# Optimization experiments

Measured on AMD Instinct MI355X. Metric: run time of the kernel, lower is better.

The kernel has to match this reference:

```python
import jax, jax.numpy as jnp
import numpy as np

NEG = -9.0e15


def setup_inputs() -> dict:
    key = jax.random.key(0)
    k_x, k_w, k_e, k_b, k_m = jax.random.split(key, 5)
    B, N, C, F = 2048, 64, 256, 256
    x = jax.random.normal(k_x, (B, N, C), dtype=jnp.float32)
    W = jax.random.normal(k_w, (2, C, F), dtype=jnp.float32) * (1.414 / np.sqrt(C + F))
    # full logit tensor; only entries where mask holds are ever read (equivalent
    # to torch's flat `e` scattered into the nonzero positions of adj)
    e = jax.random.normal(k_e, (F, N, N), dtype=jnp.float32)
    bias = jax.random.normal(k_b, (F,), dtype=jnp.float32) * (1.0 / np.sqrt(C))
    # symmetric adjacency mask with self-loops, density ~0.3
    m = jax.random.bernoulli(k_m, 0.3, (N, N))
    mask = (m | m.T) | jnp.eye(N, dtype=bool)
    return {"x": x, "W": W, "e": e, "bias": bias, "mask": mask}


def reference(x, W, e, bias, mask):
    # x: [B,N,C], W: [2,C,F], e: [F,N,N], bias: [F], mask: [N,N] bool
    h0 = x @ W[0]                                   # [B,N,F] (self term)
    h1 = x @ W[1]                                   # [B,N,F] (neighbor term)
    logits = jnp.where(mask[None, :, :], e, NEG)    # [F,N,N]
    adj = jax.nn.softmax(logits, axis=2)            # per-channel row softmax
    N = mask.shape[0]
    eye = jnp.eye(N, dtype=bool)
    d = jnp.diagonal(adj, axis1=1, axis2=2)         # [F,N]  (adj * E diagonal)
    off = jnp.where(eye[None, :, :], 0.0, adj)      # [F,N,N] (adj * (1-E))
    # (adj*E) @ h0 reduces to per-node diagonal scaling; off-diag is a
    # per-channel NxN matmul batched over B.
    out = d.T[None, :, :] * h0 + jnp.einsum('fnm,bmf->bnf', off, h1)
    return out + bias[None, None, :]
```

## Files before the change

### kernel.cpp

```cpp
#include <hip/hip_runtime.h>
#include <hip/hip_bf16.h>


typedef __attribute__((ext_vector_type(8))) short  fragA;
typedef __attribute__((ext_vector_type(4))) float  f32x4;
typedef __attribute__((ext_vector_type(8))) unsigned short u16x8;
typedef __attribute__((ext_vector_type(4))) unsigned short u16x4;

constexpr long OFF_OFF = 0;
constexpr long OFF_WT  = 2l * 1024 * 1024;
constexpr long OFF_DS  = OFF_WT + 512l * 256 * 2;
constexpr long OFF_H1  = OFF_DS + 64l * 256 * 4;
constexpr long WS_NEED = OFF_H1 + 256l * 131072 * 2;

static __device__ inline unsigned short f2bf(float f) {
  __hip_bfloat16 h = __float2bfloat16(f);
  return __builtin_bit_cast(unsigned short, h);
}
static __device__ inline float bf2f(unsigned short u) {
  unsigned int x = ((unsigned int)u) << 16;
  return __builtin_bit_cast(float, x);
}

__global__ __launch_bounds__(256) void k_prep(const float* __restrict__ e,
                                              const unsigned char* __restrict__ mask,
                                              char* __restrict__ ws_b) {
  unsigned short* off = (unsigned short*)(ws_b + OFF_OFF);
  float* dscale = (float*)(ws_b + OFF_DS);
  const int lane = threadIdx.x & 63;
  const int row  = blockIdx.x * 4 + (threadIdx.x >> 6);
  const int f = row >> 6, n = row & 63;

  bool is_u8 = __all(mask[lane * 65] != 0);
  bool mv;
  if (is_u8) mv = mask[n * 64 + lane] != 0;
  else       mv = ((const int*)mask)[n * 64 + lane] != 0;

  float v = mv ? e[(long)row * 64 + lane] : -1e30f;
  float mx = v;
#pragma unroll
  for (int s = 32; s; s >>= 1) mx = fmaxf(mx, __shfl_xor(mx, s));
  float ex = mv ? __expf(v - mx) : 0.f;
  float sm = ex;
#pragma unroll
  for (int s = 32; s; s >>= 1) sm += __shfl_xor(sm, s);
  float adj = ex / sm;
  if (lane == n) dscale[n * 256 + f] = adj;
  off[(long)row * 64 + lane] = f2bf(lane == n ? 0.f : adj);
}

__global__ __launch_bounds__(256) void k_wt(const float* __restrict__ W,
                                            char* __restrict__ ws_b) {
  unsigned short* Wt = (unsigned short*)(ws_b + OFF_WT);
  __shared__ float t[64][65];
  const int bid = blockIdx.x;
  const int w = bid >> 4, f0 = ((bid >> 2) & 3) * 64, c0 = (bid & 3) * 64;
  const int tr = threadIdx.x >> 2, tc = (threadIdx.x & 3) * 16;
  const float* src = W + ((long)(w * 256 + c0 + tr)) * 256 + f0 + tc;
#pragma unroll
  for (int i = 0; i < 16; i += 4) {
    float4 v = *(const float4*)(src + i);
    t[tr][tc + i] = v.x; t[tr][tc + i + 1] = v.y;
    t[tr][tc + i + 2] = v.z; t[tr][tc + i + 3] = v.w;
  }
  __syncthreads();
  u16x8 p0, p1;
#pragma unroll
  for (int i = 0; i < 8; i++)  p0[i] = f2bf(t[tc + i][tr]);
#pragma unroll
  for (int i = 0; i < 8; i++)  p1[i] = f2bf(t[tc + 8 + i][tr]);
  unsigned short* dst = Wt + ((long)(w * 256 + f0 + tr)) * 256 + c0 + tc;
  *(u16x8*)dst = p0;
  *(u16x8*)(dst + 8) = p1;
}

__global__ __launch_bounds__(512) void k_gemm(const float* __restrict__ x,
                                              const float* __restrict__ bias,
                                              char* __restrict__ ws_b,
                                              float* __restrict__ out) {
  const unsigned short* Wt = (const unsigned short*)(ws_b + OFF_WT);
  const float* dscale = (const float*)(ws_b + OFF_DS);
  __shared__ __align__(16) unsigned short smem[256 * 136];
  unsigned short* As = smem;
  unsigned short* Bs = smem + 128 * 72;

  const int tid  = threadIdx.x;
  const int bcol = blockIdx.x;
  const long R0  = (long)blockIdx.y * 128;
  const int wid  = tid >> 6, lane = tid & 63;
  const int wr = wid & 1, wc = wid >> 1;
  const int lr = lane & 15, lkb = (lane >> 4) * 8;

  f32x4 acc[4][4] = {};

  for (int k0 = 0; k0 < 256; k0 += 64) {
    {
      int r = tid >> 2, cb = (tid & 3) * 16;
      const float* src = x + (R0 + r) * 256 + k0 + cb;
      float4 v0 = ((const float4*)src)[0];
      float4 v1 = ((const float4*)src)[1];
      float4 v2 = ((const float4*)src)[2];
      float4 v3 = ((const float4*)src)[3];
      u16x8 p0, p1;
      p0[0]=f2bf(v0.x); p0[1]=f2bf(v0.y); p0[2]=f2bf(v0.z); p0[3]=f2bf(v0.w);
      p0[4]=f2bf(v1.x); p0[5]=f2bf(v1.y); p0[6]=f2bf(v1.z); p0[7]=f2bf(v1.w);
      p1[0]=f2bf(v2.x); p1[1]=f2bf(v2.y); p1[2]=f2bf(v2.z); p1[3]=f2bf(v2.w);
      p1[4]=f2bf(v3.x); p1[5]=f2bf(v3.y); p1[6]=f2bf(v3.z); p1[7]=f2bf(v3.w);
      unsigned short* d = As + r * 72 + cb;
      *(u16x8*)d = p0;
      *(u16x8*)(d + 8) = p1;
    }
    {
      int j = tid >> 1, cb = (tid & 1) * 32;
      const unsigned short* src = Wt + ((long)(bcol * 256 + j)) * 256 + k0 + cb;
      unsigned short* d = Bs + j * 72 + cb;
      *(u16x8*)(d)      = *(const u16x8*)(src);
      *(u16x8*)(d + 8)  = *(const u16x8*)(src + 8);
      *(u16x8*)(d + 16) = *(const u16x8*)(src + 16);
      *(u16x8*)(d + 24) = *(const u16x8*)(src + 24);
    }
    __syncthreads();
#pragma unroll
    for (int kk = 0; kk < 2; kk++) {
      fragA af[4], bfm[4];
#pragma unroll
      for (int i = 0; i < 4; i++)
        af[i] = *(const fragA*)(As + (wr * 64 + i * 16 + lr) * 72 + kk * 32 + lkb);
#pragma unroll
      for (int j = 0; j < 4; j++)
        bfm[j] = *(const fragA*)(Bs + (wc * 64 + j * 16 + lr) * 72 + kk * 32 + lkb);
#pragma unroll
      for (int i = 0; i < 4; i++)
#pragma unroll
        for (int j = 0; j < 4; j++)
          acc[i][j] = __builtin_amdgcn_mfma_f32_16x16x32_bf16(af[i], bfm[j], acc[i][j], 0, 0, 0);
    }
    __syncthreads();
  }

  if (bcol == 0) {
#pragma unroll
    for (int i = 0; i < 4; i++) {
#pragma unroll
      for (int j = 0; j < 4; j++) {
        int f = wc * 64 + j * 16 + lr;
        float bs = bias[f];
#pragma unroll
        for (int r = 0; r < 4; r++) {
          long R = R0 + wr * 64 + i * 16 + (lane >> 4) * 4 + r;
          int n = (int)(R & 63);
          out[R * 256 + f] = acc[i][j][r] * dscale[n * 256 + f] + bs;
        }
      }
    }
  } else {
    unsigned short* Ts = smem;
#pragma unroll
    for (int i = 0; i < 4; i++) {
#pragma unroll
      for (int j = 0; j < 4; j++) {
        int fl = wc * 64 + j * 16 + lr;
        int rb = wr * 64 + i * 16 + (lane >> 4) * 4;
        u16x4 pk;
        pk[0] = f2bf(acc[i][j][0]); pk[1] = f2bf(acc[i][j][1]);
        pk[2] = f2bf(acc[i][j][2]); pk[3] = f2bf(acc[i][j][3]);
        *(u16x4*)(Ts + fl * 136 + rb) = pk;
      }
    }
    __syncthreads();
    unsigned short* h1ws = (unsigned short*)(ws_b + OFF_H1);
    int fl = tid >> 1, rb2 = (tid & 1) * 64;
    unsigned short* dst = h1ws + (long)fl * 131072 + R0 + rb2;
    const unsigned short* s = Ts + fl * 136 + rb2;
#pragma unroll
    for (int i = 0; i < 8; i++)
      *(u16x8*)(dst + i * 8) = *(const u16x8*)(s + i * 8);
  }
}

__global__ __launch_bounds__(256) void k_einsum(char* __restrict__ ws_b,
                                                float* __restrict__ out) {
  const unsigned short* offp = (const unsigned short*)(ws_b + OFF_OFF);
  const unsigned short* h1ws = (const unsigned short*)(ws_b + OFF_H1);
  __shared__ __align__(16) unsigned short Ds[16 * 64 * 24];
  const int tid = threadIdx.x;
  const long B0 = (long)blockIdx.x * 16;
  const int f0 = blockIdx.y * 16;
  const int wid = tid >> 6, lane = tid & 63;
  const int lr = lane & 15, lkb = (lane >> 4) * 8;

  for (int q = 0; q < 4; q++) {
    int fi = wid * 4 + q;
    long f = f0 + fi;
    f32x4 acc[4] = {};
    const unsigned short* ha = h1ws + f * 131072 + (B0 + lr) * 64;
    const unsigned short* ob = offp + f * 4096;
#pragma unroll
    for (int kt = 0; kt < 2; kt++) {
      fragA a = *(const fragA*)(ha + kt * 32 + lkb);
#pragma unroll
      for (int ct = 0; ct < 4; ct++) {
        fragA b = *(const fragA*)(ob + (ct * 16 + lr) * 64 + kt * 32 + lkb);
        acc[ct] = __builtin_amdgcn_mfma_f32_16x16x32_bf16(a, b, acc[ct], 0, 0, 0);
      }
    }
#pragma unroll
    for (int ct = 0; ct < 4; ct++) {
      int n = ct * 16 + lr;
#pragma unroll
      for (int r = 0; r < 4; r++) {
        int b = (lane >> 4) * 4 + r;
        Ds[(b * 64 + n) * 24 + fi] = f2bf(acc[ct][r]);
      }
    }
  }
  __syncthreads();
#pragma unroll
  for (int i = 0; i < 4; i++) {
    int r = tid + 256 * i;
    float* o = out + (B0 * 64 + r) * 256 + f0;
    const unsigned short* ds = Ds + r * 24;
    u16x8 d0 = *(const u16x8*)(ds);
    u16x8 d1 = *(const u16x8*)(ds + 8);
    float4 o0 = ((float4*)o)[0], o1 = ((float4*)o)[1];
    float4 o2 = ((float4*)o)[2], o3 = ((float4*)o)[3];
    o0.x += bf2f(d0[0]); o0.y += bf2f(d0[1]); o0.z += bf2f(d0[2]); o0.w += bf2f(d0[3]);
    o1.x += bf2f(d0[4]); o1.y += bf2f(d0[5]); o1.z += bf2f(d0[6]); o1.w += bf2f(d0[7]);
    o2.x += bf2f(d1[0]); o2.y += bf2f(d1[1]); o2.z += bf2f(d1[2]); o2.w += bf2f(d1[3]);
    o3.x += bf2f(d1[4]); o3.y += bf2f(d1[5]); o3.z += bf2f(d1[6]); o3.w += bf2f(d1[7]);
    ((float4*)o)[0] = o0; ((float4*)o)[1] = o1;
    ((float4*)o)[2] = o2; ((float4*)o)[3] = o3;
  }
}

extern "C" void kernel_launch(void* const* d_in, const int* in_sizes, int n_in,
                              void* d_out, int out_size, void* d_ws, size_t ws_size,
                              hipStream_t stream) {
  const float* x    = (const float*)d_in[0];
  const float* W    = (const float*)d_in[1];
  const float* e    = (const float*)d_in[2];
  const float* bias = (const float*)d_in[3];
  const unsigned char* mask = (const unsigned char*)d_in[4];
  float* out = (float*)d_out;
  char* ws = (char*)d_ws;
  if (ws_size < (size_t)WS_NEED) return;

  k_prep<<<4096, 256, 0, stream>>>(e, mask, ws);
  k_wt<<<32, 256, 0, stream>>>(W, ws);
  dim3 g2(2, 1024);
  k_gemm<<<g2, 512, 0, stream>>>(x, bias, ws, out);
  dim3 g3(128, 16);
  k_einsum<<<g3, 256, 0, stream>>>(ws, out);
}
```

Baseline: 241.8 us.

## Fuse projection GEMM and per-channel einsum into one kernel keeping h1 in LDS

```diff
diff --git a/kernel.cpp b/kernel.cpp
--- a/kernel.cpp
+++ b/kernel.cpp
@@ -10,8 +10,7 @@
 constexpr long OFF_OFF = 0;
 constexpr long OFF_WT  = 2l * 1024 * 1024;
 constexpr long OFF_DS  = OFF_WT + 512l * 256 * 2;
-constexpr long OFF_H1  = OFF_DS + 64l * 256 * 4;
-constexpr long WS_NEED = OFF_H1 + 256l * 131072 * 2;
+constexpr long WS_NEED = OFF_DS + 64l * 256 * 4;
 
 static __device__ inline unsigned short f2bf(float f) {
   __hip_bfloat16 h = __float2bfloat16(f);
@@ -29,7 +28,7 @@
   float* dscale = (float*)(ws_b + OFF_DS);
   const int lane = threadIdx.x & 63;
   const int row  = blockIdx.x * 4 + (threadIdx.x >> 6);
-  const int f = row >> 6, n = row & 63;
+  const int n = row & 63;
 
   bool is_u8 = __all(mask[lane * 65] != 0);
   bool mv;
@@ -45,6 +44,7 @@
 #pragma unroll
   for (int s = 32; s; s >>= 1) sm += __shfl_xor(sm, s);
   float adj = ex / sm;
+  const int f = row >> 6;
   if (lane == n) dscale[n * 256 + f] = adj;
   off[(long)row * 64 + lane] = f2bf(lane == n ? 0.f : adj);
 }
@@ -74,162 +74,123 @@
   *(u16x8*)(dst + 8) = p1;
 }
 
-__global__ __launch_bounds__(512) void k_gemm(const float* __restrict__ x,
-                                              const float* __restrict__ bias,
-                                              char* __restrict__ ws_b,
-                                              float* __restrict__ out) {
-  const unsigned short* Wt = (const unsigned short*)(ws_b + OFF_WT);
-  const float* dscale = (const float*)(ws_b + OFF_DS);
-  __shared__ __align__(16) unsigned short smem[256 * 136];
-  unsigned short* As = smem;
-  unsigned short* Bs = smem + 128 * 72;
-
-  const int tid  = threadIdx.x;
-  const int bcol = blockIdx.x;
-  const long R0  = (long)blockIdx.y * 128;
-  const int wid  = tid >> 6, lane = tid & 63;
-  const int wr = wid & 1, wc = wid >> 1;
-  const int lr = lane & 15, lkb = (lane >> 4) * 8;
+__global__ __launch_bounds__(512, 4) void k_main(const float* __restrict__ x,
+                                                 const float* __restrict__ bias,
+                                                 const char* __restrict__ ws_b,
+                                                 float* __restrict__ out) {
+  const unsigned short* Wt   = (const unsigned short*)(ws_b + OFF_WT);
+  const unsigned short* offp = (const unsigned short*)(ws_b + OFF_OFF);
+  const float* dscale        = (const float*)(ws_b + OFF_DS);
+
+  __shared__ __align__(16) unsigned short Bs[64 * 264];
+  __shared__ __align__(16) unsigned short Hb[19264];
+
+  const int tid = threadIdx.x;
+  const int wid = tid >> 6, lane = tid & 63;
+  const int lr = lane & 15, hi = lane >> 4;
+
+  const int wg = blockIdx.x;
+  const int xcd = wg & 7, s = wg >> 3;
+  const int bb = xcd * 32 + (s >> 3);
+  const int fb = s & 7;
+  const int f0 = fb * 32;
+  const long R0 = (long)bb * 512;
+  const long Rw = R0 + wid * 64;
+
+  {
+    int c = tid >> 3, ch = (tid & 7) * 32;
+    int wrow = (c < 32) ? (f0 + c) : (256 + f0 + c - 32);
+    const unsigned short* src = Wt + (long)wrow * 256 + ch;
+    unsigned short* d = &Bs[c * 264 + ch];
+    *(u16x8*)(d)      = *(const u16x8*)(src);
+    *(u16x8*)(d + 8)  = *(const u16x8*)(src + 8);
+    *(u16x8*)(d + 16) = *(const u16x8*)(src + 16);
+    *(u16x8*)(d + 24) = *(const u16x8*)(src + 24);
+  }
+  __syncthreads();
 
   f32x4 acc[4][4] = {};
-
-  for (int k0 = 0; k0 < 256; k0 += 64) {
-    {
-      int r = tid >> 2, cb = (tid & 3) * 16;
-      const float* src = x + (R0 + r) * 256 + k0 + cb;
-      float4 v0 = ((const float4*)src)[0];
-      float4 v1 = ((const float4*)src)[1];
-      float4 v2 = ((const float4*)src)[2];
-      float4 v3 = ((const float4*)src)[3];
-      u16x8 p0, p1;
-      p0[0]=f2bf(v0.x); p0[1]=f2bf(v0.y); p0[2]=f2bf(v0.z); p0[3]=f2bf(v0.w);
-      p0[4]=f2bf(v1.x); p0[5]=f2bf(v1.y); p0[6]=f2bf(v1.z); p0[7]=f2bf(v1.w);
-      p1[0]=f2bf(v2.x); p1[1]=f2bf(v2.y); p1[2]=f2bf(v2.z); p1[3]=f2bf(v2.w);
-      p1[4]=f2bf(v3.x); p1[5]=f2bf(v3.y); p1[6]=f2bf(v3.z); p1[7]=f2bf(v3.w);
-      unsigned short* d = As + r * 72 + cb;
-      *(u16x8*)d = p0;
-      *(u16x8*)(d + 8) = p1;
-    }
-    {
-      int j = tid >> 1, cb = (tid & 1) * 32;
-      const unsigned short* src = Wt + ((long)(bcol * 256 + j)) * 256 + k0 + cb;
-      unsigned short* d = Bs + j * 72 + cb;
-      *(u16x8*)(d)      = *(const u16x8*)(src);
-      *(u16x8*)(d + 8)  = *(const u16x8*)(src + 8);
-      *(u16x8*)(d + 16) = *(const u16x8*)(src + 16);
-      *(u16x8*)(d + 24) = *(const u16x8*)(src + 24);
-    }
-    __syncthreads();
+#pragma unroll
+  for (int ks = 0; ks < 8; ks++) {
+    fragA af[4], bfr[4];
+#pragma unroll
+    for (int i = 0; i < 4; i++) {
+      const float* p = x + (Rw + i * 16 + lr) * 256 + ks * 32 + hi * 8;
+      float4 v0 = *(const float4*)p;
+      float4 v1 = *(const float4*)(p + 4);
+      u16x8 t;
+      t[0] = f2bf(v0.x); t[1] = f2bf(v0.y); t[2] = f2bf(v0.z); t[3] = f2bf(v0.w);
+      t[4] = f2bf(v1.x); t[5] = f2bf(v1.y); t[6] = f2bf(v1.z); t[7] = f2bf(v1.w);
+      af[i] = __builtin_bit_cast(fragA, t);
+    }
+#pragma unroll
+    for (int j = 0; j < 4; j++)
+      bfr[j] = *(const fragA*)&Bs[(j * 16 + lr) * 264 + ks * 32 + hi * 8];
+#pragma unroll
+    for (int i = 0; i < 4; i++)
+#pragma unroll
+      for (int j = 0; j < 4; j++)
+        acc[i][j] = __builtin_amdgcn_mfma_f32_16x16x32_bf16(af[i], bfr[j], acc[i][j], 0, 0, 0);
+  }
+
+#pragma unroll
+  for (int i = 0; i < 4; i++) {
+#pragma unroll
+    for (int j = 2; j < 4; j++) {
+      int fl = (j - 2) * 16 + lr;
+      int m  = i * 16 + hi * 4;
+      u16x4 pk;
+      pk[0] = f2bf(acc[i][j][0]); pk[1] = f2bf(acc[i][j][1]);
+      pk[2] = f2bf(acc[i][j][2]); pk[3] = f2bf(acc[i][j][3]);
+      *(u16x4*)&Hb[fl * 584 + wid * 72 + m] = pk;
+    }
+  }
+  __syncthreads();
+
+#pragma unroll
+  for (int q = 0; q < 4; q++) {
+    int fl = wid * 4 + q;
+    long fg = f0 + fl;
+    f32x4 ea[4] = {};
+    const unsigned short* ob = offp + fg * 4096;
 #pragma unroll
     for (int kk = 0; kk < 2; kk++) {
-      fragA af[4], bfm[4];
-#pragma unroll
-      for (int i = 0; i < 4; i++)
-        af[i] = *(const fragA*)(As + (wr * 64 + i * 16 + lr) * 72 + kk * 32 + lkb);
-#pragma unroll
-      for (int j = 0; j < 4; j++)
-        bfm[j] = *(const fragA*)(Bs + (wc * 64 + j * 16 + lr) * 72 + kk * 32 + lkb);
-#pragma unroll
-      for (int i = 0; i < 4; i++)
-#pragma unroll
-        for (int j = 0; j < 4; j++)
-          acc[i][j] = __builtin_amdgcn_mfma_f32_16x16x32_bf16(af[i], bfm[j], acc[i][j], 0, 0, 0);
-    }
-    __syncthreads();
-  }
-
-  if (bcol == 0) {
-#pragma unroll
-    for (int i = 0; i < 4; i++) {
-#pragma unroll
-      for (int j = 0; j < 4; j++) {
-        int f = wc * 64 + j * 16 + lr;
-        float bs = bias[f];
+      fragA a = *(const fragA*)&Hb[fl * 584 + lr * 72 + kk * 32 + hi * 8];
+#pragma unroll
+      for (int ct = 0; ct < 4; ct++) {
+        fragA b = *(const fragA*)(ob + (ct * 16 + lr) * 64 + kk * 32 + hi * 8);
+        ea[ct] = __builtin_amdgcn_mfma_f32_16x16x32_bf16(a, b, ea[ct], 0, 0, 0);
+      }
+    }
+    if (hi < 2) {
+#pragma unroll
+      for (int ct = 0; ct < 4; ct++) {
 #pragma unroll
         for (int r = 0; r < 4; r++) {
-          long R = R0 + wr * 64 + i * 16 + (lane >> 4) * 4 + r;
-          int n = (int)(R & 63);
-          out[R * 256 + f] = acc[i][j][r] * dscale[n * 256 + f] + bs;
+          int b = hi * 4 + r;
+          int n = ct * 16 + lr;
+          Hb[fl * 584 + b * 72 + n] = f2bf(ea[ct][r]);
         }
       }
     }
-  } else {
-    unsigned short* Ts = smem;
-#pragma unroll
-    for (int i = 0; i < 4; i++) {
-#pragma unroll
-      for (int j = 0; j < 4; j++) {
-        int fl = wc * 64 + j * 16 + lr;
-        int rb = wr * 64 + i * 16 + (lane >> 4) * 4;
-        u16x4 pk;
-        pk[0] = f2bf(acc[i][j][0]); pk[1] = f2bf(acc[i][j][1]);
-        pk[2] = f2bf(acc[i][j][2]); pk[3] = f2bf(acc[i][j][3]);
-        *(u16x4*)(Ts + fl * 136 + rb) = pk;
+  }
+  __syncthreads();
+
+#pragma unroll
+  for (int i = 0; i < 4; i++) {
+#pragma unroll
+    for (int j = 0; j < 2; j++) {
+      int fl = j * 16 + lr;
+      int f  = f0 + fl;
+      float bs = bias[f];
+#pragma unroll
+      for (int r = 0; r < 4; r++) {
+        int m = i * 16 + hi * 4 + r;
+        float ev = bf2f(Hb[fl * 584 + wid * 72 + m]);
+        long R = Rw + m;
+        out[R * 256 + f] = dscale[m * 256 + f] * acc[i][j][r] + ev + bs;
       }
     }
-    __syncthreads();
-    unsigned short* h1ws = (unsigned short*)(ws_b + OFF_H1);
-    int fl = tid >> 1, rb2 = (tid & 1) * 64;
-    unsigned short* dst = h1ws + (long)fl * 131072 + R0 + rb2;
-    const unsigned short* s = Ts + fl * 136 + rb2;
-#pragma unroll
-    for (int i = 0; i < 8; i++)
-      *(u16x8*)(dst + i * 8) = *(const u16x8*)(s + i * 8);
-  }
-}
-
-__global__ __launch_bounds__(256) void k_einsum(char* __restrict__ ws_b,
-                                                float* __restrict__ out) {
-  const unsigned short* offp = (const unsigned short*)(ws_b + OFF_OFF);
-  const unsigned short* h1ws = (const unsigned short*)(ws_b + OFF_H1);
-  __shared__ __align__(16) unsigned short Ds[16 * 64 * 24];
-  const int tid = threadIdx.x;
-  const long B0 = (long)blockIdx.x * 16;
-  const int f0 = blockIdx.y * 16;
-  const int wid = tid >> 6, lane = tid & 63;
-  const int lr = lane & 15, lkb = (lane >> 4) * 8;
-
-  for (int q = 0; q < 4; q++) {
-    int fi = wid * 4 + q;
-    long f = f0 + fi;
-    f32x4 acc[4] = {};
-    const unsigned short* ha = h1ws + f * 131072 + (B0 + lr) * 64;
-    const unsigned short* ob = offp + f * 4096;
-#pragma unroll
-    for (int kt = 0; kt < 2; kt++) {
-      fragA a = *(const fragA*)(ha + kt * 32 + lkb);
-#pragma unroll
-      for (int ct = 0; ct < 4; ct++) {
-        fragA b = *(const fragA*)(ob + (ct * 16 + lr) * 64 + kt * 32 + lkb);
-        acc[ct] = __builtin_amdgcn_mfma_f32_16x16x32_bf16(a, b, acc[ct], 0, 0, 0);
-      }
-    }
-#pragma unroll
-    for (int ct = 0; ct < 4; ct++) {
-      int n = ct * 16 + lr;
-#pragma unroll
-      for (int r = 0; r < 4; r++) {
-        int b = (lane >> 4) * 4 + r;
-        Ds[(b * 64 + n) * 24 + fi] = f2bf(acc[ct][r]);
-      }
-    }
-  }
-  __syncthreads();
-#pragma unroll
-  for (int i = 0; i < 4; i++) {
-    int r = tid + 256 * i;
-    float* o = out + (B0 * 64 + r) * 256 + f0;
-    const unsigned short* ds = Ds + r * 24;
-    u16x8 d0 = *(const u16x8*)(ds);
-    u16x8 d1 = *(const u16x8*)(ds + 8);
-    float4 o0 = ((float4*)o)[0], o1 = ((float4*)o)[1];
-    float4 o2 = ((float4*)o)[2], o3 = ((float4*)o)[3];
-    o0.x += bf2f(d0[0]); o0.y += bf2f(d0[1]); o0.z += bf2f(d0[2]); o0.w += bf2f(d0[3]);
-    o1.x += bf2f(d0[4]); o1.y += bf2f(d0[5]); o1.z += bf2f(d0[6]); o1.w += bf2f(d0[7]);
-    o2.x += bf2f(d1[0]); o2.y += bf2f(d1[1]); o2.z += bf2f(d1[2]); o2.w += bf2f(d1[3]);
-    o3.x += bf2f(d1[4]); o3.y += bf2f(d1[5]); o3.z += bf2f(d1[6]); o3.w += bf2f(d1[7]);
-    ((float4*)o)[0] = o0; ((float4*)o)[1] = o1;
-    ((float4*)o)[2] = o2; ((float4*)o)[3] = o3;
   }
 }
 
@@ -247,8 +208,5 @@
 
   k_prep<<<4096, 256, 0, stream>>>(e, mask, ws);
   k_wt<<<32, 256, 0, stream>>>(W, ws);
-  dim3 g2(2, 1024);
-  k_gemm<<<g2, 512, 0, stream>>>(x, bias, ws, out);
-  dim3 g3(128, 16);
-  k_einsum<<<g3, 256, 0, stream>>>(ws, out);
-}
+  k_main<<<2048, 512, 0, stream>>>(x, bias, ws, out);
+}
```

Result: faster. 205.5 us (-15.0%).
